# Performance work log

Measured on AMD Instinct MI355X. Metric: run time of the kernel, lower is better.

The kernel has to match this reference:

```python
import jax, jax.numpy as jnp
from jax import lax
import numpy as np

V, E = 50000, 300          # word vocab / embedding dim
CV, CE = 200, 30           # char vocab / char embed dim
NF = 50                    # conv filters per kernel size
KS = (2, 3, 4)
H = 512                    # lstm hidden per direction
T = 20                     # num tags
B, S, C = 32, 256, 16      # batch, seq len, max chars per word
PAD = 0


def setup_inputs() -> dict:
    key = jax.random.key(0)
    ks = jax.random.split(key, 24)
    pos = jnp.arange(S)
    lengths = jax.random.randint(ks[0], (B,), S // 2, S + 1)
    mask = pos[None, :] < lengths[:, None]
    x = jnp.where(mask, jax.random.randint(ks[1], (B, S), 1, V), 0).astype(jnp.int32)
    x_chars = jnp.where(mask[:, :, None], jax.random.randint(ks[2], (B, S, C), 1, CV), 0).astype(jnp.int32)
    tags = jnp.where(mask, jax.random.randint(ks[3], (B, S), 1, T), 0).astype(jnp.int32)
    n = lambda k, sh, s=0.1: s * jax.random.normal(k, sh, jnp.float32)
    IN0 = E + NF * len(KS)  # 450 = lstm layer-0 input size
    return dict(
        x=x, x_chars=x_chars, tags=tags,
        word_embed=n(ks[4], (V, E)).at[PAD].set(0.0),
        char_embed=n(ks[5], (CV, CE)).at[0].set(0.0),
        conv_w2=n(ks[6], (NF, CE, 2)), conv_b2=n(ks[7], (NF,)),
        conv_w3=n(ks[8], (NF, CE, 3)), conv_b3=n(ks[9], (NF,)),
        conv_w4=n(ks[10], (NF, CE, 4)), conv_b4=n(ks[11], (NF,)),
        l0_wih=n(ks[12], (2, 4 * H, IN0), 0.04), l0_whh=n(ks[13], (2, 4 * H, H), 0.04),
        l0_bih=n(ks[14], (2, 4 * H), 0.04), l0_bhh=jnp.zeros((2, 4 * H), jnp.float32),
        l1_wih=n(ks[15], (2, 4 * H, 2 * H), 0.03), l1_whh=n(ks[16], (2, 4 * H, H), 0.03),
        l1_bih=n(ks[17], (2, 4 * H), 0.03), l1_bhh=jnp.zeros((2, 4 * H), jnp.float32),
        hw_Hw=n(ks[18], (2 * H, 2 * H), 0.02), hw_Hb=jnp.zeros((2 * H,), jnp.float32),
        hw_Tw=n(ks[19], (2 * H, 2 * H), 0.02), hw_Tb=-jnp.ones((2 * H,), jnp.float32),
        fc_w=n(ks[20], (T, 2 * H), 0.05), fc_b=jnp.zeros((T,), jnp.float32),
        crf_start=n(ks[21], (T,)), crf_end=n(ks[22], (T,)), crf_trans=n(ks[23], (T, T)),
    )


def _char_cnn(x_chars, char_embed, convs):
    b, s, c = x_chars.shape
    emb = char_embed[x_chars.reshape(b * s, c)].transpose(0, 2, 1)  # (B*S, CE, C)
    pooled = []
    for w, bias in convs:
        o = lax.conv_general_dilated(emb, w, (1,), 'VALID', dimension_numbers=('NCH', 'OIH', 'NCH'))
        pooled.append(jnp.max(jax.nn.relu(o + bias[None, :, None]), axis=-1))  # (B*S, NF)
    return jnp.concatenate(pooled, -1).reshape(b, s, -1)


def _lstm_dir(xs, wih, whh, bih, bhh, reverse):
    # xs: (S, B, in). PyTorch gate order: i, f, g, o.
    b = xs.shape[1]
    h = whh.shape[-1]
    bias = bih + bhh

    def step(carry, xt):
        hp, cp = carry
        g = xt @ wih.T + hp @ whh.T + bias
        i, f, gg, o = jnp.split(g, 4, axis=-1)
        cn = jax.nn.sigmoid(f) * cp + jax.nn.sigmoid(i) * jnp.tanh(gg)
        hn = jax.nn.sigmoid(o) * jnp.tanh(cn)
        return (hn, cn), hn

    init = (jnp.zeros((b, h), xs.dtype), jnp.zeros((b, h), xs.dtype))
    _, hs = lax.scan(step, init, xs, reverse=reverse)
    return hs  # (S, B, H), time-aligned with xs


def _bilstm_layer(xs, wih, whh, bih, bhh):
    fwd = _lstm_dir(xs, wih[0], whh[0], bih[0], bhh[0], False)
    bwd = _lstm_dir(xs, wih[1], whh[1], bih[1], bhh[1], True)
    return jnp.concatenate([fwd, bwd], axis=-1)


def _forward(x, x_chars, tags, word_embed, char_embed,
             conv_w2, conv_b2, conv_w3, conv_b3, conv_w4, conv_b4,
             l0_wih, l0_whh, l0_bih, l0_bhh, l1_wih, l1_whh, l1_bih, l1_bhh,
             hw_Hw, hw_Hb, hw_Tw, hw_Tb, fc_w, fc_b,
             crf_start, crf_end, crf_trans):
    mask = x != PAD  # (B, S)
    # ----- encoder (dropout = identity in eval) -----
    w_emb = word_embed[x]                              # (B, S, E)
    c_emb = _char_cnn(x_chars, char_embed,
                      [(conv_w2, conv_b2), (conv_w3, conv_b3), (conv_w4, conv_b4)])
    combined = jnp.concatenate([w_emb, c_emb], -1)     # (B, S, E+150)
    xs = combined.transpose(1, 0, 2)                   # (S, B, in)
    xs = _bilstm_layer(xs, l0_wih, l0_whh, l0_bih, l0_bhh)
    xs = _bilstm_layer(xs, l1_wih, l1_whh, l1_bih, l1_bhh)
    out = xs.transpose(1, 0, 2)                        # (B, S, 2H)
    t_gate = jax.nn.sigmoid(out @ hw_Tw.T + hw_Tb)
    out = t_gate * jax.nn.relu(out @ hw_Hw.T + hw_Hb) + (1.0 - t_gate) * out
    logits = out @ fc_w.T + fc_b                       # (B, S, T)

    # ----- CRF negative log-likelihood (torchcrf, reduction='mean') -----
    b, s, t = logits.shape
    maskf = mask.astype(logits.dtype)
    em_scores = jnp.take_along_axis(logits, tags[..., None], axis=-1)[..., 0]  # (B, S)
    trans_scores = crf_trans[tags[:, :-1], tags[:, 1:]]                        # (B, S-1)
    score = crf_start[tags[:, 0]] + em_scores[:, 0]
    score = score + jnp.sum(maskf[:, 1:] * (trans_scores + em_scores[:, 1:]), axis=1)
    last_idx = jnp.sum(mask, axis=1) - 1
    last_tags = tags[jnp.arange(b), last_idx]
    score = score + crf_end[last_tags]

    def fwd_step(alpha, inp):
        em_t, m_t = inp  # (B, T), (B,)
        nxt = jax.nn.logsumexp(alpha[:, :, None] + crf_trans[None] + em_t[:, None, :], axis=1)
        return jnp.where(m_t[:, None], nxt, alpha), None

    alpha0 = crf_start[None, :] + logits[:, 0]
    alpha, _ = lax.scan(fwd_step, alpha0,
                        (logits[:, 1:].transpose(1, 0, 2), mask[:, 1:].T))
    log_z = jax.nn.logsumexp(alpha + crf_end[None, :], axis=1)
    crf_loss = -jnp.mean(score - log_z)

    # ----- aux CE loss (ignore_index = PAD) -----
    lp = jax.nn.log_softmax(logits.reshape(b * s, t), axis=-1)
    nll = -jnp.take_along_axis(lp, tags.reshape(b * s, 1), axis=-1)[:, 0]
    valid = (tags.reshape(b * s) != PAD).astype(logits.dtype)
    aux = jnp.sum(nll * valid) / jnp.sum(valid)

    return crf_loss + 0.1 * aux


def reference(x, x_chars, tags, word_embed, char_embed,
              conv_w2, conv_b2, conv_w3, conv_b3, conv_w4, conv_b4,
              l0_wih, l0_whh, l0_bih, l0_bhh, l1_wih, l1_whh, l1_bih, l1_bhh,
              hw_Hw, hw_Hb, hw_Tw, hw_Tb, fc_w, fc_b,
              crf_start, crf_end, crf_trans):
    return _forward(x, x_chars, tags, word_embed, char_embed,
                    conv_w2, conv_b2, conv_w3, conv_b3, conv_w4, conv_b4,
                    l0_wih, l0_whh, l0_bih, l0_bhh, l1_wih, l1_whh, l1_bih, l1_bhh,
                    hw_Hw, hw_Hb, hw_Tw, hw_Tb, fc_w, fc_b,
                    crf_start, crf_end, crf_trans)
```

## Files before the change

kernel.cpp:

```cpp
#include <hip/hip_runtime.h>
#include <math.h>

#define B_   32
#define S_   256
#define T_   20
#define H_   512
#define E_   300
#define C_   16
#define CE_  30
#define NF_  50
#define IN0_ 450
#define KP0_ 480
#define G4_  2048
#define NG_  4096

typedef __attribute__((ext_vector_type(8))) short bf16x8;
typedef __attribute__((ext_vector_type(4))) float f32x4;

__device__ __forceinline__ float sigm(float x) { return 1.f / (1.f + __expf(-x)); }
__device__ __forceinline__ float tanhfast(float x) {
  x = fminf(15.f, fmaxf(-15.f, x));
  float e = __expf(-2.f * x);
  return (1.f - e) / (1.f + e);
}
__device__ __forceinline__ unsigned short f2bf(float f) {
  unsigned int u = __float_as_uint(f);
  unsigned int r = (u + 0x7fffu + ((u >> 16) & 1u)) >> 16;
  return (unsigned short)r;
}
__device__ __forceinline__ float bf2f(unsigned int u) {
  return __uint_as_float(u << 16);
}

#define GLOAD_LDS(gp, lp)                                                    \
  __builtin_amdgcn_global_load_lds(                                          \
      (const __attribute__((address_space(1))) void*)(gp),                   \
      (__attribute__((address_space(3))) void*)(lp), 16, 0, 0)

__global__ __launch_bounds__(256) void embed_cnn(
    const int* __restrict__ x, const int* __restrict__ xc,
    const float* __restrict__ wemb, const float* __restrict__ cemb,
    const float* __restrict__ w2, const float* __restrict__ cb2,
    const float* __restrict__ w3, const float* __restrict__ cb3,
    const float* __restrict__ w4, const float* __restrict__ cb4,
    unsigned short* __restrict__ out) {
  int m = blockIdx.x;
  int t = m >> 5, b = m & 31;
  int tid = threadIdx.x;
  __shared__ float emb[C_][CE_];
  __shared__ float conv[2100];

  int wid = x[b * S_ + t];
  for (int e = tid; e < KP0_; e += 256) {
    if (e < E_) out[(size_t)m * KP0_ + e] = f2bf(wemb[(size_t)wid * E_ + e]);
    else if (e >= IN0_) out[(size_t)m * KP0_ + e] = 0;
  }

  for (int idx = tid; idx < C_ * CE_; idx += 256) {
    int c = idx / CE_, ce = idx % CE_;
    int cid = xc[(b * S_ + t) * C_ + c];
    emb[c][ce] = cemb[cid * CE_ + ce];
  }
  __syncthreads();

  for (int idx = tid; idx < 2100; idx += 256) {
    int kw, f, p;
    const float* w; const float* bb;
    int r = idx;
    if (r < 750)      { kw = 2; f = r / 15; p = r % 15; w = w2; bb = cb2; }
    else if (r < 1450){ r -= 750;  kw = 3; f = r / 14; p = r % 14; w = w3; bb = cb3; }
    else              { r -= 1450; kw = 4; f = r / 13; p = r % 13; w = w4; bb = cb4; }
    float acc = bb[f];
    for (int j = 0; j < kw; ++j)
      for (int ce = 0; ce < CE_; ++ce)
        acc = fmaf(emb[p + j][ce], w[(f * CE_ + ce) * kw + j], acc);
    conv[idx] = fmaxf(acc, 0.f);
  }
  __syncthreads();

  if (tid < 150) {
    int kk = tid / 50, f = tid % 50;
    int base, np;
    if (kk == 0)      { base = f * 15;        np = 15; }
    else if (kk == 1) { base = 750 + f * 14;  np = 14; }
    else              { base = 1450 + f * 13; np = 13; }
    float mx = 0.f;
    for (int p = 0; p < np; ++p) mx = fmaxf(mx, conv[base + p]);
    out[(size_t)m * KP0_ + E_ + kk * 50 + f] = f2bf(mx);
  }
}

__global__ __launch_bounds__(256) void castpad(
    const float* __restrict__ src, unsigned short* __restrict__ dst,
    int R, int K, int Kp) {
  int i = blockIdx.x * 256 + threadIdx.x;
  if (i < R * Kp) {
    int r = i / Kp, k = i - r * Kp;
    dst[i] = (k < K) ? f2bf(src[(size_t)r * K + k]) : (unsigned short)0;
  }
}

__global__ __launch_bounds__(256) void gemm_bf16(
    const unsigned short* __restrict__ A, const unsigned short* __restrict__ W,
    const float* __restrict__ bias1, const float* __restrict__ bias2,
    float* __restrict__ C, int M, int N, int Kp) {
  __shared__ unsigned short As[128][32];
  __shared__ unsigned short Bs[128][32];
  int bm = blockIdx.y * 128, bn = blockIdx.x * 128;
  int tid = threadIdx.x;
  int wave = tid >> 6, lane = tid & 63;
  int wm = (wave & 1) * 64, wn = (wave >> 1) * 64;
  int l15 = lane & 15, l4 = lane >> 4;

  int srow = lane >> 2;
  int scol = (lane & 3) * 8;
  const unsigned short* ga0 = A + (size_t)(bm + wave * 32 + srow) * Kp + scol;
  const unsigned short* ga1 = A + (size_t)(bm + wave * 32 + 16 + srow) * Kp + scol;
  const unsigned short* gb0 = W + (size_t)(bn + wave * 32 + srow) * Kp + scol;
  const unsigned short* gb1 = W + (size_t)(bn + wave * 32 + 16 + srow) * Kp + scol;

  f32x4 acc[4][4];
#pragma unroll
  for (int i = 0; i < 4; ++i)
#pragma unroll
    for (int j = 0; j < 4; ++j) acc[i][j] = (f32x4){0.f, 0.f, 0.f, 0.f};

  for (int k0 = 0; k0 < Kp; k0 += 32) {
    __syncthreads();
    GLOAD_LDS(ga0 + k0, &As[wave * 32][0]);
    GLOAD_LDS(ga1 + k0, &As[wave * 32 + 16][0]);
    GLOAD_LDS(gb0 + k0, &Bs[wave * 32][0]);
    GLOAD_LDS(gb1 + k0, &Bs[wave * 32 + 16][0]);
    __syncthreads();

    bf16x8 af[4], bfv[4];
#pragma unroll
    for (int i = 0; i < 4; ++i) af[i]  = *(const bf16x8*)&As[wm + i * 16 + l15][l4 * 8];
#pragma unroll
    for (int j = 0; j < 4; ++j) bfv[j] = *(const bf16x8*)&Bs[wn + j * 16 + l15][l4 * 8];
#pragma unroll
    for (int i = 0; i < 4; ++i)
#pragma unroll
      for (int j = 0; j < 4; ++j)
        acc[i][j] = __builtin_amdgcn_mfma_f32_16x16x32_bf16(af[i], bfv[j], acc[i][j], 0, 0, 0);
  }

#pragma unroll
  for (int j = 0; j < 4; ++j) {
    int gn = bn + wn + j * 16 + l15;
    float bsum = (bias1 ? bias1[gn] : 0.f) + (bias2 ? bias2[gn] : 0.f);
#pragma unroll
    for (int i = 0; i < 4; ++i) {
#pragma unroll
      for (int r = 0; r < 4; ++r) {
        int gm = bm + wm + i * 16 + l4 * 4 + r;
        C[(size_t)gm * N + gn] = acc[i][j][r] + bsum;
      }
    }
  }
}

__global__ __launch_bounds__(512, 2) void lstm_scan(
    const float* __restrict__ P,
    const float* __restrict__ whh,
    unsigned short* __restrict__ Hbf,
    unsigned int* __restrict__ hT,
    int* __restrict__ flags) {
  int wg  = blockIdx.x;
  int dir = wg >> 5;
  int hb  = wg & 31;
  int tid = threadIdx.x;
  int wave = tid >> 6;
  int lane = tid & 63;
  int g  = wave & 3;
  int nb = wave >> 2;
  int l15 = lane & 15;
  int l4  = lane >> 4;

  int grow = g * H_ + hb * 16 + l15;
  const float* wrow = whh + ((size_t)dir * G4_ + grow) * H_;
  bf16x8 afrag[16];
#pragma unroll
  for (int kk = 0; kk < 16; ++kk) {
    int k0 = kk * 32 + l4 * 8;
    float4 lo = *(const float4*)(wrow + k0);
    float4 hi = *(const float4*)(wrow + k0 + 4);
    bf16x8 a;
    a[0] = (short)f2bf(lo.x); a[1] = (short)f2bf(lo.y);
    a[2] = (short)f2bf(lo.z); a[3] = (short)f2bf(lo.w);
    a[4] = (short)f2bf(hi.x); a[5] = (short)f2bf(hi.y);
    a[6] = (short)f2bf(hi.z); a[7] = (short)f2bf(hi.w);
    afrag[kk] = a;
  }

  __shared__ float lds_g[4][16][32];
  __shared__ unsigned short hlds[32][520];
  int* dflags = flags + dir * 32;

  bool pw = tid < 256;
  int pb = tid & 31, pq = (tid >> 5) & 7;
  float c0 = 0.f, c1 = 0.f;
  float2 pfc[4], pfn[4];

  {
    int t0i = dir ? (S_ - 1) : 0;
    if (pw) {
      size_t pr = ((size_t)(t0i * B_ + pb)) * NG_ + (size_t)dir * G4_ + hb * 16 + 2 * pq;
#pragma unroll
      for (int gg = 0; gg < 4; ++gg) pfc[gg] = *(const float2*)(P + pr + gg * H_);
    }
  }

  int srow   = wave * 4 + (lane & 3);
  int schunk = lane >> 2;
  const unsigned short* slabBase = (const unsigned short*)hT + (size_t)dir * (32 * 512);

  for (int s = 0; s < S_; ++s) {
    int t = dir ? (S_ - 1 - s) : s;

    f32x4 acc = {0.f, 0.f, 0.f, 0.f};
    if (s > 0) {
      const unsigned short* src = slabBase + (size_t)((s + 1) & 1) * (2 * 32 * 512)
                                  + srow * 512 + schunk * 32;
      bf16x8 t0, t1, t2, t3;
      asm volatile("global_load_dwordx4 %0, %1, off sc0 sc1"           : "=v"(t0) : "v"(src) : "memory");
      asm volatile("global_load_dwordx4 %0, %1, off offset:16 sc0 sc1" : "=v"(t1) : "v"(src) : "memory");
      asm volatile("global_load_dwordx4 %0, %1, off offset:32 sc0 sc1" : "=v"(t2) : "v"(src) : "memory");
      asm volatile("global_load_dwordx4 %0, %1, off offset:48 sc0 sc1" : "=v"(t3) : "v"(src) : "memory");
      if (pw && s < S_ - 1) {
        int tn = dir ? (S_ - 2 - s) : (s + 1);
        size_t pr = ((size_t)(tn * B_ + pb)) * NG_ + (size_t)dir * G4_ + hb * 16 + 2 * pq;
#pragma unroll
        for (int gg = 0; gg < 4; ++gg) pfn[gg] = *(const float2*)(P + pr + gg * H_);
        asm volatile("s_waitcnt vmcnt(4)" ::: "memory");
      } else {
        asm volatile("s_waitcnt vmcnt(0)" ::: "memory");
      }
      __builtin_amdgcn_sched_barrier(0);
      *(bf16x8*)&hlds[srow][schunk * 32 +  0] = t0;
      *(bf16x8*)&hlds[srow][schunk * 32 +  8] = t1;
      *(bf16x8*)&hlds[srow][schunk * 32 + 16] = t2;
      *(bf16x8*)&hlds[srow][schunk * 32 + 24] = t3;
      __syncthreads();

      bf16x8 bv[16];
#pragma unroll
      for (int kk = 0; kk < 16; ++kk)
        bv[kk] = *(const bf16x8*)&hlds[nb * 16 + l15][kk * 32 + l4 * 8];
#pragma unroll
      for (int kk = 0; kk < 16; ++kk)
        acc = __builtin_amdgcn_mfma_f32_16x16x32_bf16(afrag[kk], bv[kk], acc, 0, 0, 0);
    } else {
      if (pw) {
        int tn = dir ? (S_ - 2) : 1;
        size_t pr = ((size_t)(tn * B_ + pb)) * NG_ + (size_t)dir * G4_ + hb * 16 + 2 * pq;
#pragma unroll
        for (int gg = 0; gg < 4; ++gg) pfn[gg] = *(const float2*)(P + pr + gg * H_);
      }
    }

#pragma unroll
    for (int r = 0; r < 4; ++r)
      lds_g[g][l4 * 4 + r][l15 + 16 * nb] = acc[r];
    __syncthreads();

    if (pw) {
      int h0 = 2 * pq, h1 = 2 * pq + 1;
      float iv0 = lds_g[0][h0][pb] + pfc[0].x, iv1 = lds_g[0][h1][pb] + pfc[0].y;
      float fv0 = lds_g[1][h0][pb] + pfc[1].x, fv1 = lds_g[1][h1][pb] + pfc[1].y;
      float gv0 = lds_g[2][h0][pb] + pfc[2].x, gv1 = lds_g[2][h1][pb] + pfc[2].y;
      float ov0 = lds_g[3][h0][pb] + pfc[3].x, ov1 = lds_g[3][h1][pb] + pfc[3].y;
      float cn0 = sigm(fv0) * c0 + sigm(iv0) * tanhfast(gv0);
      float cn1 = sigm(fv1) * c1 + sigm(iv1) * tanhfast(gv1);
      float hn0 = sigm(ov0) * tanhfast(cn0);
      float hn1 = sigm(ov1) * tanhfast(cn1);
      c0 = cn0; c1 = cn1;
      unsigned int hp = (unsigned int)f2bf(hn0) | ((unsigned int)f2bf(hn1) << 16);
      *(unsigned int*)(Hbf + ((size_t)(t * B_ + pb)) * 1024 + dir * H_ + hb * 16 + 2 * pq) = hp;
      unsigned int* hc = hT + ((((size_t)(s & 1) * 2 + dir) * 32 + pb) * 256 + hb * 8 + pq);
      __hip_atomic_store(hc, hp, __ATOMIC_RELAXED, __HIP_MEMORY_SCOPE_AGENT);
#pragma unroll
      for (int gg = 0; gg < 4; ++gg) pfc[gg] = pfn[gg];
    }

    if (s < S_ - 1) {
      __syncthreads();
      if (wave == 0) {
        int target = s + 1;
        if (lane == 0)
          __hip_atomic_store(dflags + hb, target, __ATOMIC_RELAXED, __HIP_MEMORY_SCOPE_AGENT);
        int guard = 0;
        for (;;) {
          int v = target;
          if (lane < 32)
            v = __hip_atomic_load(dflags + lane, __ATOMIC_RELAXED, __HIP_MEMORY_SCOPE_AGENT);
          if (__all(v >= target)) break;
          __builtin_amdgcn_s_sleep(1);
          if (++guard > (1 << 17)) break;
        }
      }
      __syncthreads();
    }
  }
}

__global__ __launch_bounds__(256) void hwfc_k(
    const unsigned int* __restrict__ Xbf,
    const float* __restrict__ G12,
    const float* __restrict__ hw_Tb, const float* __restrict__ hw_Hb,
    const float* __restrict__ fc_w,
    const float* __restrict__ fc_b,
    float* __restrict__ LOG) {
  int m = blockIdx.x;
  int tid = threadIdx.x;
  int wave = tid >> 6, lane = tid & 63;
  int e0 = tid * 4;

  unsigned int xv0 = Xbf[(size_t)m * 512 + tid * 2];
  unsigned int xv1 = Xbf[(size_t)m * 512 + tid * 2 + 1];
  float4 g1 = *(const float4*)(G12 + (size_t)m * 2048 + e0);
  float4 g2 = *(const float4*)(G12 + (size_t)m * 2048 + 1024 + e0);
  float4 tb = *(const float4*)(hw_Tb + e0);
  float4 hbv = *(const float4*)(hw_Hb + e0);
  g1.x += tb.x; g1.y += tb.y; g1.z += tb.z; g1.w += tb.w;
  g2.x += hbv.x; g2.y += hbv.y; g2.z += hbv.z; g2.w += hbv.w;
  float tg, o[4];
  tg = sigm(g1.x); o[0] = tg * fmaxf(g2.x, 0.f) + (1.f - tg) * bf2f(xv0 & 0xffffu);
  tg = sigm(g1.y); o[1] = tg * fmaxf(g2.y, 0.f) + (1.f - tg) * bf2f(xv0 >> 16);
  tg = sigm(g1.z); o[2] = tg * fmaxf(g2.z, 0.f) + (1.f - tg) * bf2f(xv1 & 0xffffu);
  tg = sigm(g1.w); o[3] = tg * fmaxf(g2.w, 0.f) + (1.f - tg) * bf2f(xv1 >> 16);

  float acc[T_];
#pragma unroll
  for (int j = 0; j < T_; ++j) {
    float4 w = *(const float4*)(fc_w + (size_t)j * 1024 + e0);
    acc[j] = o[0] * w.x + o[1] * w.y + o[2] * w.z + o[3] * w.w;
  }
#pragma unroll
  for (int off = 32; off > 0; off >>= 1)
#pragma unroll
    for (int j = 0; j < T_; ++j)
      acc[j] += __shfl_xor(acc[j], off);

  __shared__ float part[4][T_];
  if (lane == 0)
#pragma unroll
    for (int j = 0; j < T_; ++j) part[wave][j] = acc[j];
  __syncthreads();
  if (tid < T_)
    LOG[(size_t)m * T_ + tid] =
        part[0][tid] + part[1][tid] + part[2][tid] + part[3][tid] + fc_b[tid];
}

__global__ __launch_bounds__(256) void crf_score_k(
    const int* __restrict__ x, const int* __restrict__ tags,
    const float* __restrict__ L,
    const float* __restrict__ cstart, const float* __restrict__ cend,
    const float* __restrict__ ctrans, float* __restrict__ score) {
  int b = blockIdx.x;
  int t = threadIdx.x;
  int tg = tags[b * S_ + t];
  float part = 0.f;
  bool valid;
  if (t == 0) {
    part = cstart[tg] + L[(size_t)b * T_ + tg];
    valid = true;
  } else {
    valid = (x[b * S_ + t] != 0);
    if (valid)
      part = ctrans[tags[b * S_ + t - 1] * T_ + tg] + L[((size_t)t * B_ + b) * T_ + tg];
  }
  bool nextInvalid = (t == S_ - 1) || (x[b * S_ + t + 1] == 0);
  if (valid && nextInvalid) part += cend[tg];

  __shared__ float red[256];
  red[t] = part;
  __syncthreads();
  for (int off = 128; off > 0; off >>= 1) {
    if (t < off) red[t] += red[t + off];
    __syncthreads();
  }
  if (t == 0) score[b] = red[0];
}

__global__ __launch_bounds__(64) void crf_forward_k(
    const int* __restrict__ x, const float* __restrict__ L,
    const float* __restrict__ cstart, const float* __restrict__ cend,
    const float* __restrict__ ctrans, float* __restrict__ logz) {
  int b = blockIdx.x;
  int tp = threadIdx.x;
  __shared__ float alpha[T_];
  __shared__ float trT[T_][T_];
  for (int i = tp; i < T_ * T_; i += 64)
    trT[i / T_][i % T_] = ctrans[(i % T_) * T_ + (i / T_)];
  if (tp < T_) alpha[tp] = cstart[tp] + L[(size_t)b * T_ + tp];
  __syncthreads();
  for (int t = 1; t < S_; ++t) {
    float newv = 0.f;
    bool active = tp < T_;
    bool msk = x[b * S_ + t] != 0;
    if (active) {
      float em = L[((size_t)t * B_ + b) * T_ + tp];
      float mx = -1e30f;
#pragma unroll
      for (int tt = 0; tt < T_; ++tt) mx = fmaxf(mx, alpha[tt] + trT[tp][tt]);
      float sum = 0.f;
#pragma unroll
      for (int tt = 0; tt < T_; ++tt) sum += __expf(alpha[tt] + trT[tp][tt] - mx);
      float nxt = mx + __logf(sum) + em;
      newv = msk ? nxt : alpha[tp];
    }
    __syncthreads();
    if (active) alpha[tp] = newv;
    __syncthreads();
  }
  if (tp == 0) {
    float mx = -1e30f;
    for (int tt = 0; tt < T_; ++tt) mx = fmaxf(mx, alpha[tt] + cend[tt]);
    float sum = 0.f;
    for (int tt = 0; tt < T_; ++tt) sum += __expf(alpha[tt] + cend[tt] - mx);
    logz[b] = mx + __logf(sum);
  }
}

__global__ __launch_bounds__(256) void nll_k(const float* __restrict__ L,
                                             const int* __restrict__ tags,
                                             float* __restrict__ accum) {
  int m = blockIdx.x * 256 + threadIdx.x;
  float nv = 0.f, vv = 0.f;
  if (m < B_ * S_) {
    int t = m >> 5, b = m & 31;
    int tg = tags[b * S_ + t];
    const float* row = L + (size_t)m * T_;
    float mx = -1e30f;
    for (int i = 0; i < T_; ++i) mx = fmaxf(mx, row[i]);
    float sum = 0.f;
    for (int i = 0; i < T_; ++i) sum += expf(row[i] - mx);
    float lse = mx + logf(sum);
    if (tg != 0) { nv = lse - row[tg]; vv = 1.f; }
  }
  __shared__ float sn[256], sv[256];
  int tid = threadIdx.x;
  sn[tid] = nv; sv[tid] = vv;
  __syncthreads();
  for (int off = 128; off > 0; off >>= 1) {
    if (tid < off) { sn[tid] += sn[tid + off]; sv[tid] += sv[tid + off]; }
    __syncthreads();
  }
  if (tid == 0) { atomicAdd(&accum[0], sn[0]); atomicAdd(&accum[1], sv[0]); }
}

__global__ void final_k(const float* __restrict__ score, const float* __restrict__ logz,
                        const float* __restrict__ accum, float* __restrict__ out) {
  if (threadIdx.x == 0 && blockIdx.x == 0) {
    float s = 0.f;
    for (int b = 0; b < B_; ++b) s += score[b] - logz[b];
    float crf = -s / (float)B_;
    out[0] = crf + 0.1f * (accum[0] / accum[1]);
  }
}

extern "C" void kernel_launch(void* const* d_in, const int* in_sizes, int n_in,
                              void* d_out, int out_size, void* d_ws, size_t ws_size,
                              hipStream_t stream) {
  (void)in_sizes; (void)n_in; (void)out_size; (void)ws_size;
  const int*   x      = (const int*)d_in[0];
  const int*   xc     = (const int*)d_in[1];
  const int*   tags   = (const int*)d_in[2];
  const float* wemb   = (const float*)d_in[3];
  const float* cemb   = (const float*)d_in[4];
  const float* w2     = (const float*)d_in[5];
  const float* cb2    = (const float*)d_in[6];
  const float* w3     = (const float*)d_in[7];
  const float* cb3    = (const float*)d_in[8];
  const float* w4     = (const float*)d_in[9];
  const float* cb4    = (const float*)d_in[10];
  const float* l0_wih = (const float*)d_in[11];
  const float* l0_whh = (const float*)d_in[12];
  const float* l0_bih = (const float*)d_in[13];
  const float* l0_bhh = (const float*)d_in[14];
  const float* l1_wih = (const float*)d_in[15];
  const float* l1_whh = (const float*)d_in[16];
  const float* l1_bih = (const float*)d_in[17];
  const float* l1_bhh = (const float*)d_in[18];
  const float* hw_Hw  = (const float*)d_in[19];
  const float* hw_Hb  = (const float*)d_in[20];
  const float* hw_Tw  = (const float*)d_in[21];
  const float* hw_Tb  = (const float*)d_in[22];
  const float* fc_w   = (const float*)d_in[23];
  const float* fc_b   = (const float*)d_in[24];
  const float* cstart = (const float*)d_in[25];
  const float* cend   = (const float*)d_in[26];
  const float* ctrans = (const float*)d_in[27];

  float* ws    = (float*)d_ws;
  float* P     = ws;
  float* G12   = P;
  unsigned short* Hbf    = (unsigned short*)(ws + 33554432);
  unsigned short* COMBbf = (unsigned short*)(ws + 37748736);
  unsigned short* Wbf    = (unsigned short*)(ws + 39714816);
  float* LOG   = ws + 41811968;
  unsigned int* hT = (unsigned int*)(ws + 41975808);
  int*   flags = (int*)(ws + 42008576);
  float* score = ws + 42008576 + 128;
  float* logz  = score + 32;
  float* accum = logz + 32;

  hipMemsetAsync(accum, 0, 2 * sizeof(float), stream);

  embed_cnn<<<B_ * S_, 256, 0, stream>>>(x, xc, wemb, cemb, w2, cb2, w3, cb3, w4, cb4, COMBbf);

  castpad<<<(4096 * KP0_ + 255) / 256, 256, 0, stream>>>(l0_wih, Wbf, 4096, IN0_, KP0_);
  {
    dim3 g(NG_ / 128, (B_ * S_) / 128);
    gemm_bf16<<<g, 256, 0, stream>>>(COMBbf, Wbf, l0_bih, l0_bhh, P, B_ * S_, NG_, KP0_);
  }
  hipMemsetAsync(flags, 0, 128 * sizeof(int), stream);
  lstm_scan<<<64, 512, 0, stream>>>(P, l0_whh, Hbf, hT, flags);

  castpad<<<(4096 * 1024 + 255) / 256, 256, 0, stream>>>(l1_wih, Wbf, 4096, 1024, 1024);
  {
    dim3 g(NG_ / 128, (B_ * S_) / 128);
    gemm_bf16<<<g, 256, 0, stream>>>(Hbf, Wbf, l1_bih, l1_bhh, P, B_ * S_, NG_, 1024);
  }
  hipMemsetAsync(flags, 0, 128 * sizeof(int), stream);
  lstm_scan<<<64, 512, 0, stream>>>(P, l1_whh, Hbf, hT, flags);

  castpad<<<(1024 * 1024 + 255) / 256, 256, 0, stream>>>(hw_Tw, Wbf, 1024, 1024, 1024);
  castpad<<<(1024 * 1024 + 255) / 256, 256, 0, stream>>>(hw_Hw, Wbf + 1024 * 1024, 1024, 1024, 1024);
  {
    dim3 g(2048 / 128, (B_ * S_) / 128);
    gemm_bf16<<<g, 256, 0, stream>>>(Hbf, Wbf, nullptr, nullptr, G12, B_ * S_, 2048, 1024);
  }
  hwfc_k<<<B_ * S_, 256, 0, stream>>>(
      (const unsigned int*)Hbf, G12, hw_Tb, hw_Hb, fc_w, fc_b, LOG);

  crf_score_k<<<B_, 256, 0, stream>>>(x, tags, LOG, cstart, cend, ctrans, score);
  crf_forward_k<<<B_, 64, 0, stream>>>(x, LOG, cstart, cend, ctrans, logz);
  nll_k<<<(B_ * S_ + 255) / 256, 256, 0, stream>>>(LOG, tags, accum);
  final_k<<<1, 64, 0, stream>>>(score, logz, accum, (float*)d_out);
}
```

Baseline: 3.396 ms.

## Interleave LSTM gate rows so each lane computes its cell update in registers

The recurrent weight rows are reordered so each MFMA output lane holds all four gates (i,f,g,o) for one hidden unit and batch element. The cell update then runs directly in registers on all waves, which removes the LDS gate staging buffer and one __syncthreads per timestep on the serial path. Adjacent hidden outputs are packed into 32-bit words with a cross-lane shuffle before the stores. P prefetches become scalar per-lane loads instead of float2 loads.

```diff
diff --git a/kernel.cpp b/kernel.cpp
--- a/kernel.cpp
+++ b/kernel.cpp
@@ -163,7 +163,7 @@
 __global__ __launch_bounds__(512, 2) void lstm_scan(
     const float* __restrict__ P,
     const float* __restrict__ whh,
-    unsigned short* __restrict__ Hbf,
+    unsigned int* __restrict__ Hbf32,
     unsigned int* __restrict__ hT,
     int* __restrict__ flags) {
   int wg  = blockIdx.x;
@@ -172,13 +172,18 @@
   int tid = threadIdx.x;
   int wave = tid >> 6;
   int lane = tid & 63;
-  int g  = wave & 3;
-  int nb = wave >> 2;
+  int hq = wave >> 1;
+  int nb = wave & 1;
   int l15 = lane & 15;
   int l4  = lane >> 4;
-
-  int grow = g * H_ + hb * 16 + l15;
-  const float* wrow = whh + ((size_t)dir * G4_ + grow) * H_;
+  int hidx = hb * 16 + hq * 4 + l4;
+  int bidx = nb * 16 + l15;
+
+  {
+  }
+  int arow_h = hb * 16 + hq * 4 + (l15 >> 2);
+  int arow_g = l15 & 3;
+  const float* wrow = whh + ((size_t)dir * G4_ + arow_g * H_ + arow_h) * H_;
   bf16x8 afrag[16];
 #pragma unroll
   for (int kk = 0; kk < 16; ++kk) {
@@ -193,22 +198,17 @@
     afrag[kk] = a;
   }
 
-  __shared__ float lds_g[4][16][32];
   __shared__ unsigned short hlds[32][520];
   int* dflags = flags + dir * 32;
 
-  bool pw = tid < 256;
-  int pb = tid & 31, pq = (tid >> 5) & 7;
-  float c0 = 0.f, c1 = 0.f;
-  float2 pfc[4], pfn[4];
+  float cst = 0.f;
+  float pfc[4], pfn[4];
 
   {
     int t0i = dir ? (S_ - 1) : 0;
-    if (pw) {
-      size_t pr = ((size_t)(t0i * B_ + pb)) * NG_ + (size_t)dir * G4_ + hb * 16 + 2 * pq;
-#pragma unroll
-      for (int gg = 0; gg < 4; ++gg) pfc[gg] = *(const float2*)(P + pr + gg * H_);
-    }
+    size_t pr = ((size_t)(t0i * B_ + bidx)) * NG_ + (size_t)dir * G4_ + hidx;
+#pragma unroll
+    for (int gg = 0; gg < 4; ++gg) pfc[gg] = P[pr + gg * H_];
   }
 
   int srow   = wave * 4 + (lane & 3);
@@ -227,11 +227,11 @@
       asm volatile("global_load_dwordx4 %0, %1, off offset:16 sc0 sc1" : "=v"(t1) : "v"(src) : "memory");
       asm volatile("global_load_dwordx4 %0, %1, off offset:32 sc0 sc1" : "=v"(t2) : "v"(src) : "memory");
       asm volatile("global_load_dwordx4 %0, %1, off offset:48 sc0 sc1" : "=v"(t3) : "v"(src) : "memory");
-      if (pw && s < S_ - 1) {
+      if (s < S_ - 1) {
         int tn = dir ? (S_ - 2 - s) : (s + 1);
-        size_t pr = ((size_t)(tn * B_ + pb)) * NG_ + (size_t)dir * G4_ + hb * 16 + 2 * pq;
-#pragma unroll
-        for (int gg = 0; gg < 4; ++gg) pfn[gg] = *(const float2*)(P + pr + gg * H_);
+        size_t pr = ((size_t)(tn * B_ + bidx)) * NG_ + (size_t)dir * G4_ + hidx;
+#pragma unroll
+        for (int gg = 0; gg < 4; ++gg) pfn[gg] = P[pr + gg * H_];
         asm volatile("s_waitcnt vmcnt(4)" ::: "memory");
       } else {
         asm volatile("s_waitcnt vmcnt(0)" ::: "memory");
@@ -251,34 +251,28 @@
       for (int kk = 0; kk < 16; ++kk)
         acc = __builtin_amdgcn_mfma_f32_16x16x32_bf16(afrag[kk], bv[kk], acc, 0, 0, 0);
     } else {
-      if (pw) {
-        int tn = dir ? (S_ - 2) : 1;
-        size_t pr = ((size_t)(tn * B_ + pb)) * NG_ + (size_t)dir * G4_ + hb * 16 + 2 * pq;
-#pragma unroll
-        for (int gg = 0; gg < 4; ++gg) pfn[gg] = *(const float2*)(P + pr + gg * H_);
+      int tn = dir ? (S_ - 2) : 1;
+      size_t pr = ((size_t)(tn * B_ + bidx)) * NG_ + (size_t)dir * G4_ + hidx;
+#pragma unroll
+      for (int gg = 0; gg < 4; ++gg) pfn[gg] = P[pr + gg * H_];
+    }
+
+    {
+      float iv = acc[0] + pfc[0];
+      float fv = acc[1] + pfc[1];
+      float gv = acc[2] + pfc[2];
+      float ov = acc[3] + pfc[3];
+      cst = sigm(fv) * cst + sigm(iv) * tanhfast(gv);
+      float hn = sigm(ov) * tanhfast(cst);
+      unsigned int m = (unsigned int)f2bf(hn);
+      unsigned int pm = (unsigned int)__shfl_xor((int)m, 16);
+      if ((l4 & 1) == 0) {
+        unsigned int w = m | (pm << 16);
+        int hw = hidx >> 1;
+        Hbf32[((size_t)(t * B_ + bidx)) * 512 + dir * 256 + hw] = w;
+        unsigned int* hc = hT + (((size_t)(s & 1) * 2 + dir) * 32 + bidx) * 256 + hw;
+        __hip_atomic_store(hc, w, __ATOMIC_RELAXED, __HIP_MEMORY_SCOPE_AGENT);
       }
-    }
-
-#pragma unroll
-    for (int r = 0; r < 4; ++r)
-      lds_g[g][l4 * 4 + r][l15 + 16 * nb] = acc[r];
-    __syncthreads();
-
-    if (pw) {
-      int h0 = 2 * pq, h1 = 2 * pq + 1;
-      float iv0 = lds_g[0][h0][pb] + pfc[0].x, iv1 = lds_g[0][h1][pb] + pfc[0].y;
-      float fv0 = lds_g[1][h0][pb] + pfc[1].x, fv1 = lds_g[1][h1][pb] + pfc[1].y;
-      float gv0 = lds_g[2][h0][pb] + pfc[2].x, gv1 = lds_g[2][h1][pb] + pfc[2].y;
-      float ov0 = lds_g[3][h0][pb] + pfc[3].x, ov1 = lds_g[3][h1][pb] + pfc[3].y;
-      float cn0 = sigm(fv0) * c0 + sigm(iv0) * tanhfast(gv0);
-      float cn1 = sigm(fv1) * c1 + sigm(iv1) * tanhfast(gv1);
-      float hn0 = sigm(ov0) * tanhfast(cn0);
-      float hn1 = sigm(ov1) * tanhfast(cn1);
-      c0 = cn0; c1 = cn1;
-      unsigned int hp = (unsigned int)f2bf(hn0) | ((unsigned int)f2bf(hn1) << 16);
-      *(unsigned int*)(Hbf + ((size_t)(t * B_ + pb)) * 1024 + dir * H_ + hb * 16 + 2 * pq) = hp;
-      unsigned int* hc = hT + ((((size_t)(s & 1) * 2 + dir) * 32 + pb) * 256 + hb * 8 + pq);
-      __hip_atomic_store(hc, hp, __ATOMIC_RELAXED, __HIP_MEMORY_SCOPE_AGENT);
 #pragma unroll
       for (int gg = 0; gg < 4; ++gg) pfc[gg] = pfn[gg];
     }
@@ -516,7 +510,7 @@
     gemm_bf16<<<g, 256, 0, stream>>>(COMBbf, Wbf, l0_bih, l0_bhh, P, B_ * S_, NG_, KP0_);
   }
   hipMemsetAsync(flags, 0, 128 * sizeof(int), stream);
-  lstm_scan<<<64, 512, 0, stream>>>(P, l0_whh, Hbf, hT, flags);
+  lstm_scan<<<64, 512, 0, stream>>>(P, l0_whh, (unsigned int*)Hbf, hT, flags);
 
   castpad<<<(4096 * 1024 + 255) / 256, 256, 0, stream>>>(l1_wih, Wbf, 4096, 1024, 1024);
   {
@@ -524,7 +518,7 @@
     gemm_bf16<<<g, 256, 0, stream>>>(Hbf, Wbf, l1_bih, l1_bhh, P, B_ * S_, NG_, 1024);
   }
   hipMemsetAsync(flags, 0, 128 * sizeof(int), stream);
-  lstm_scan<<<64, 512, 0, stream>>>(P, l1_whh, Hbf, hT, flags);
+  lstm_scan<<<64, 512, 0, stream>>>(P, l1_whh, (unsigned int*)Hbf, hT, flags);
 
   castpad<<<(1024 * 1024 + 255) / 256, 256, 0, stream>>>(hw_Tw, Wbf, 1024, 1024, 1024);
   castpad<<<(1024 * 1024 + 255) / 256, 256, 0, stream>>>(hw_Hw, Wbf + 1024 * 1024, 1024, 1024, 1024);
```

After: 3.289 ms. 3.1% less time.
